# Performance work log

Measured on AMD Instinct MI355X. Metric: run time of the kernel, lower is better.

Reference implementation:

```python
import jax, jax.numpy as jnp
import numpy as np

KSIZE = 5      # equivalent steerable kernel size
KMAX = 3       # max circular harmonic
STRIDE = 2
N_IN, N_OUT = 32, 16
B_TOTAL = 3 + 2 * KMAX  # 3 radial atoms at k=0, 2 per harmonic k>=1


def _make_basis():
    # Radial steerable base: Gaussian rings x circular harmonics cos(k*theta)/sin(k*theta)
    ys, xs = np.mgrid[:KSIZE, :KSIZE].astype(np.float64) - (KSIZE - 1) / 2
    r = np.sqrt(xs ** 2 + ys ** 2)
    th = np.arctan2(ys, xs)
    ring = lambda r0: np.exp(-(r - r0) ** 2 / (2 * 0.6 ** 2))
    b0 = np.stack([ring(r0) for r0 in (0.0, 1.0, 2.0)])          # (3, 5, 5)
    br, bi = [], []
    for k in range(1, KMAX + 1):
        br.append(np.stack([ring(r0) * np.cos(k * th) for r0 in (1.0, 2.0)]))  # (2,5,5)
        bi.append(np.stack([ring(r0) * np.sin(k * th) for r0 in (1.0, 2.0)]))
    return (b0.astype(np.float32),
            [b.astype(np.float32) for b in br],
            [b.astype(np.float32) for b in bi])


def _conv_transpose(x, w):
    # torch conv_transpose2d (stride=2, padding='same' -> pad=2, output_padding=1)
    # == dilated-input conv with spatially flipped kernel, explicit pad (2,3).
    rhs = jnp.flip(w, axis=(2, 3))  # (o, i, kh, kw)
    return jax.lax.conv_general_dilated(
        x, rhs, window_strides=(1, 1), padding=((2, 3), (2, 3)),
        lhs_dilation=(STRIDE, STRIDE),
        dimension_numbers=('NCHW', 'OIHW', 'NCHW'))


def setup_inputs() -> dict:
    key = jax.random.key(0)
    k1, k2, k3, k4 = jax.random.split(key, 4)
    x = jax.random.normal(k1, (8, N_IN, 192, 192), jnp.float32)
    # alpha[0]=cos-like, alpha[1]=sin-like field at output resolution; not unit-norm,
    # rho is derived from its norm (rho=None path of forward()).
    alpha = jax.random.normal(k2, (2, 8, 1, 384, 384), jnp.float32)
    weights = jax.random.normal(k3, (N_OUT, N_IN, B_TOTAL), jnp.float32) / np.sqrt(N_IN * B_TOTAL)
    bias = jax.random.normal(k4, (N_OUT,), jnp.float32) * 0.05
    return {"x": x, "alpha": alpha, "weights": weights, "bias": bias}


def reference(x, alpha, weights, bias):
    b0, br, bi = _make_basis()
    # normalize_vector: rho = |alpha|, alpha <- alpha / rho
    rho = jnp.sqrt(jnp.sum(alpha * alpha, axis=0))          # (b, 1, Ho, Wo)
    au = alpha / (rho[None] + 1e-8)
    c1, s1 = au[0], au[1]                                    # cos(a), sin(a)
    # k=0 term (rotation invariant)
    out = _conv_transpose(x, jnp.einsum('oib,bhw->oihw', weights[:, :, :3], jnp.asarray(b0)))
    ck, sk = c1, s1
    off = 3
    for k in range(KMAX):  # harmonics k=1..KMAX, steered by cos(k a), sin(k a)
        wk = weights[:, :, off:off + 2]
        off += 2
        Kr = jnp.einsum('oib,bhw->oihw', wk, jnp.asarray(br[k]))
        Ki = jnp.einsum('oib,bhw->oihw', wk, jnp.asarray(bi[k]))
        out = out + _conv_transpose(x, Kr) * ck + _conv_transpose(x, Ki) * sk
        ckn = ck * c1 - sk * s1  # Chebyshev-style recurrence for cos/sin of (k+1)a
        skn = sk * c1 + ck * s1
        ck, sk = ckn, skn
    return rho * out + bias[None, :, None, None]
```

## Files before the change

### kernel.cpp

```cpp
#include <hip/hip_runtime.h>

#define HIN 192
#define WOUT 384
#define NIN 32
#define NOUT 16
#define NSLOT 9
#define HP 194
#define HPLANE (HP * HP)
#define HQBATCH ((size_t)HPLANE * 18)

typedef float v2f __attribute__((ext_vector_type(2)));

__device__ __forceinline__ unsigned short f2bf(float f) {
    union { float f; unsigned int u; } v; v.f = f;
    unsigned int r = v.u + 0x7fffu + ((v.u >> 16) & 1u);
    return (unsigned short)(r >> 16);
}
__device__ __forceinline__ v2f up2(unsigned u) {
    v2f r;
    r.x = __uint_as_float(u << 16);
    r.y = __uint_as_float(u & 0xffff0000u);
    return r;
}

__global__ __launch_bounds__(256) void kprep_w(const float* __restrict__ w, float* __restrict__ Wt) {
    int t = blockIdx.x * 256 + threadIdx.x;
    if (t >= NIN * NSLOT * NOUT) return;
    int c = t >> 8, r = t & 255;
    int i = r >> 3, j = r & 7;
    int m = c * 8 + j;
    int s = m >> 4, o = m & 15;
    Wt[t] = w[(o * NIN + i) * NSLOT + s];
}

__global__ __launch_bounds__(256) void kzero(uint4* __restrict__ hq, int nb) {
    int t = blockIdx.x * 256 + threadIdx.x;
    if (t >= nb * 772) return;
    int b = t / 772, r = t % 772;
    int iy, ix;
    if (r < 194)      { iy = 0;           ix = r; }
    else if (r < 388) { iy = 193;         ix = r - 194; }
    else if (r < 580) { iy = r - 388 + 1; ix = 0; }
    else              { iy = r - 580 + 1; ix = 193; }
    uint4* p = hq + (size_t)b * HQBATCH + iy * HP + ix;
    uint4 z; z.x = 0; z.y = 0; z.z = 0; z.w = 0;
    #pragma unroll
    for (int c = 0; c < 18; ++c) p[(size_t)c * HPLANE] = z;
}

__global__ __launch_bounds__(256) void kA(const float* __restrict__ x,
                                          const float* __restrict__ Wt,
                                          uint4* __restrict__ hq, int n0) {
    const int b = blockIdx.y;
    const int n = n0 + b;
    const int px = blockIdx.x * 256 + threadIdx.x;
    const int iy = px / HIN, ix = px % HIN;
    const float* xp = x + (size_t)n * NIN * HIN * HIN + px;
    float xv[NIN];
    #pragma unroll
    for (int i = 0; i < NIN; ++i) xv[i] = xp[(size_t)i * HIN * HIN];
    const int pos = (iy + 1) * HP + (ix + 1);
    uint4* hb = hq + (size_t)b * HQBATCH;
    #pragma unroll 1
    for (int c = 0; c < 18; ++c) {
        const float* wc = Wt + c * 256;
        float a[8];
        #pragma unroll
        for (int j = 0; j < 8; ++j) a[j] = 0.0f;
        #pragma unroll
        for (int i = 0; i < NIN; ++i) {
            const float xi = xv[i];
            #pragma unroll
            for (int j = 0; j < 8; ++j) a[j] = fmaf(wc[i * 8 + j], xi, a[j]);
        }
        uint4 v;
        v.x = (unsigned)f2bf(a[0]) | ((unsigned)f2bf(a[1]) << 16);
        v.y = (unsigned)f2bf(a[2]) | ((unsigned)f2bf(a[3]) << 16);
        v.z = (unsigned)f2bf(a[4]) | ((unsigned)f2bf(a[5]) << 16);
        v.w = (unsigned)f2bf(a[6]) | ((unsigned)f2bf(a[7]) << 16);
        hb[(size_t)c * HPLANE + pos] = v;
    }
}

template<int PY, int PX, int HF>
__device__ __forceinline__ void kb_body(const uint4* __restrict__ hb,
                                        const float* __restrict__ alpha,
                                        const float* __restrict__ bias_,
                                        float (&stage)[2][16][128],
                                        const float2 (&Cb)[NSLOT][25],
                                        int n, int Y, int X, int lane) {
    const int oy = 2 * Y + PY, ox = 2 * X + PX;
    const int aoff = (n * WOUT + oy) * WOUT + ox;
    const float a0 = alpha[aoff];
    const float a1 = alpha[(size_t)8 * WOUT * WOUT + aoff];
    const float rr = sqrtf(a0 * a0 + a1 * a1);
    const float inv = 1.0f / (rr + 1e-8f);
    float cc[3], ss[3];
    cc[0] = a0 * inv;                      ss[0] = a1 * inv;
    cc[1] = cc[0] * cc[0] - ss[0] * ss[0]; ss[1] = 2.0f * cc[0] * ss[0];
    cc[2] = cc[1] * cc[0] - ss[1] * ss[0]; ss[2] = ss[1] * cc[0] + cc[1] * ss[0];

    v2f acc2[4];
    #pragma unroll
    for (int j = 0; j < 4; ++j) { acc2[j].x = 0.0f; acc2[j].y = 0.0f; }

    #pragma unroll 1
    for (int ty = 0; ty < 3 - PY; ++ty) {
        const int piy = Y + 2 - ty;
        #pragma unroll 1
        for (int tx = 0; tx < 3 - PX; ++tx) {
            const int pix = X + 2 - tx;
            const int bi = (PY + 2 * ty) * 5 + (PX + 2 * tx);
            const unsigned pos = (unsigned)(piy * HP + pix);
            #pragma unroll
            for (int s = 0; s < NSLOT; ++s) {
                const float2 C = Cb[s][bi];
                float eb;
                if      (s < 3) eb = C.x;
                else if (s < 5) eb = C.x * cc[0] + C.y * ss[0];
                else if (s < 7) eb = C.x * cc[1] + C.y * ss[1];
                else            eb = C.x * cc[2] + C.y * ss[2];
                const uint4 v = hb[(size_t)(2 * s + HF) * HPLANE + pos];
                v2f e2; e2.x = eb; e2.y = eb;
                acc2[0] += e2 * up2(v.x);
                acc2[1] += e2 * up2(v.y);
                acc2[2] += e2 * up2(v.z);
                acc2[3] += e2 * up2(v.w);
            }
        }
    }

    #pragma unroll
    for (int j = 0; j < 4; ++j) {
        stage[PY][HF * 8 + 2 * j + 0][2 * lane + PX] = rr * acc2[j].x + bias_[HF * 8 + 2 * j + 0];
        stage[PY][HF * 8 + 2 * j + 1][2 * lane + PX] = rr * acc2[j].y + bias_[HF * 8 + 2 * j + 1];
    }
}

__global__ __launch_bounds__(512, 4) void kB(const uint4* __restrict__ hq,
                                             const float* __restrict__ alpha,
                                             const float* __restrict__ bias,
                                             float* __restrict__ out, int n0, int nb) {
    __shared__ float2 Cb[NSLOT][25];
    __shared__ float stage[2][16][128];
    {
        const int q = threadIdx.x;
        if (q < NSLOT * 25) {
            int s = q / 25, p = q % 25;
            int ky = p / 5, kx = p % 5;
            float ys = (float)(ky - 2), xs = (float)(kx - 2);
            float r = sqrtf(xs * xs + ys * ys);
            float th = atan2f(ys, xs);
            float cr, ci;
            if (s < 3) {
                float d = r - (float)s;
                cr = expf(-d * d * (1.0f / 0.72f));
                ci = 0.0f;
            } else {
                int k = (s - 3) / 2 + 1;
                float r0 = ((s - 3) & 1) ? 2.0f : 1.0f;
                float d = r - r0;
                float ring = expf(-d * d * (1.0f / 0.72f));
                float a = (float)k * th;
                cr = ring * cosf(a);
                ci = ring * sinf(a);
            }
            Cb[s][p] = make_float2(cr, ci);
        }
    }
    __syncthreads();

    const int tot = gridDim.x;
    const int cpx = tot >> 3;
    const int swz = ((int)blockIdx.x & 7) * cpx + ((int)blockIdx.x >> 3);
    const int Y = swz % 192;
    const int rest = swz / 192;
    const int b = rest % nb;
    const int bx = rest / nb;

    const int n = n0 + b;
    const int lane = threadIdx.x & 63;
    const int wv = threadIdx.x >> 6;
    const int X0 = bx * 64;
    const int X = X0 + lane;
    const uint4* hb = hq + (size_t)b * HQBATCH;

    switch (wv) {
        case 0: kb_body<0, 0, 0>(hb, alpha, bias, stage, Cb, n, Y, X, lane); break;
        case 1: kb_body<0, 1, 0>(hb, alpha, bias, stage, Cb, n, Y, X, lane); break;
        case 2: kb_body<1, 0, 0>(hb, alpha, bias, stage, Cb, n, Y, X, lane); break;
        case 3: kb_body<1, 1, 0>(hb, alpha, bias, stage, Cb, n, Y, X, lane); break;
        case 4: kb_body<0, 0, 1>(hb, alpha, bias, stage, Cb, n, Y, X, lane); break;
        case 5: kb_body<0, 1, 1>(hb, alpha, bias, stage, Cb, n, Y, X, lane); break;
        case 6: kb_body<1, 0, 1>(hb, alpha, bias, stage, Cb, n, Y, X, lane); break;
        default: kb_body<1, 1, 1>(hb, alpha, bias, stage, Cb, n, Y, X, lane); break;
    }

    __syncthreads();

    #pragma unroll
    for (int q = 0; q < 8; ++q) {
        const int f = q * 512 + threadIdx.x;
        const int row = f >> 7, col = f & 127;
        const int py = row >> 4, o = row & 15;
        out[(((size_t)n * NOUT + o) * WOUT + (2 * Y + py)) * WOUT + 2 * X0 + col]
            = stage[py][o][col];
    }
}

__global__ __launch_bounds__(256) void steered_convT(
    const float* __restrict__ x, const float* __restrict__ alpha,
    const float* __restrict__ weights, const float* __restrict__ bias,
    float* __restrict__ out) {
    __shared__ float sb[15 * 25];
    for (int q = threadIdx.x; q < 375; q += 256) {
        int s = q / 25, p = q % 25;
        int ky = p / 5, kx = p % 5;
        float ys = (float)(ky - 2), xs = (float)(kx - 2);
        float r = sqrtf(xs * xs + ys * ys);
        float th = atan2f(ys, xs);
        float val;
        if (s < 3) { float d = r - (float)s; val = expf(-d * d * (1.0f / 0.72f)); }
        else {
            int k = (s - 3) / 4 + 1; int rem = (s - 3) & 3;
            float r0 = (rem & 1) ? 2.0f : 1.0f; float d = r - r0;
            float ring = expf(-d * d * (1.0f / 0.72f));
            float ang = (float)k * th;
            val = ring * ((rem < 2) ? cosf(ang) : sinf(ang));
        }
        sb[q] = val;
    }
    __syncthreads();
    int idx = blockIdx.x * 256 + threadIdx.x;
    int ox = idx % WOUT; int tt = idx / WOUT; int oy = tt % WOUT; int n = tt / WOUT;
    const int plane = WOUT * WOUT;
    int aoff = (n * WOUT + oy) * WOUT + ox;
    float a0 = alpha[aoff], a1 = alpha[8 * plane + aoff];
    float rho = sqrtf(a0 * a0 + a1 * a1);
    float inv = 1.0f / (rho + 1e-8f);
    float c1 = a0 * inv, s1 = a1 * inv;
    float c2 = c1 * c1 - s1 * s1, s2 = 2.0f * s1 * c1;
    float c3 = c2 * c1 - s2 * s1, s3 = s2 * c1 + c2 * s1;
    int py = oy & 1, px = ox & 1;
    int iy0 = (oy >> 1) + 1, ix0 = (ox >> 1) + 1;
    float eb[9][9]; int off[9];
    #pragma unroll
    for (int t = 0; t < 9; ++t) {
        int ty = t / 3, tx = t % 3;
        int ky = py + 2 * ty, kx = px + 2 * tx;
        int iy = iy0 - ty, ix = ix0 - tx;
        bool v = (ky < 5) && (kx < 5) && (iy >= 0) && (iy < HIN) && (ix >= 0) && (ix < HIN);
        float m = v ? 1.0f : 0.0f;
        int ciy = min(max(iy, 0), HIN - 1), cix = min(max(ix, 0), HIN - 1);
        off[t] = ciy * HIN + cix;
        int bi_ = min(ky, 4) * 5 + min(kx, 4);
        eb[0][t] = sb[0 * 25 + bi_] * m;
        eb[1][t] = sb[1 * 25 + bi_] * m;
        eb[2][t] = sb[2 * 25 + bi_] * m;
        eb[3][t] = (sb[3 * 25 + bi_] * c1 + sb[5 * 25 + bi_] * s1) * m;
        eb[4][t] = (sb[4 * 25 + bi_] * c1 + sb[6 * 25 + bi_] * s1) * m;
        eb[5][t] = (sb[7 * 25 + bi_] * c2 + sb[9 * 25 + bi_] * s2) * m;
        eb[6][t] = (sb[8 * 25 + bi_] * c2 + sb[10 * 25 + bi_] * s2) * m;
        eb[7][t] = (sb[11 * 25 + bi_] * c3 + sb[13 * 25 + bi_] * s3) * m;
        eb[8][t] = (sb[12 * 25 + bi_] * c3 + sb[14 * 25 + bi_] * s3) * m;
    }
    float acc[NOUT];
    #pragma unroll
    for (int o = 0; o < NOUT; ++o) acc[o] = 0.0f;
    const float* xn = x + (size_t)n * NIN * HIN * HIN;
    for (int i = 0; i < NIN; ++i) {
        const float* xp = xn + (size_t)i * HIN * HIN;
        float tap[9];
        #pragma unroll
        for (int t = 0; t < 9; ++t) tap[t] = xp[off[t]];
        float G[9];
        #pragma unroll
        for (int b = 0; b < 9; ++b) {
            float s = 0.0f;
            #pragma unroll
            for (int t = 0; t < 9; ++t) s += eb[b][t] * tap[t];
            G[b] = s;
        }
        const float* wp = weights + i * 9;
        #pragma unroll
        for (int o = 0; o < NOUT; ++o) {
            float s = acc[o];
            #pragma unroll
            for (int b = 0; b < 9; ++b) s += wp[o * NIN * 9 + b] * G[b];
            acc[o] = s;
        }
    }
    #pragma unroll
    for (int o = 0; o < NOUT; ++o)
        out[((size_t)(n * NOUT + o) * WOUT + oy) * WOUT + ox] = rho * acc[o] + bias[o];
}

extern "C" void kernel_launch(void* const* d_in, const int* in_sizes, int n_in,
                              void* d_out, int out_size, void* d_ws, size_t ws_size,
                              hipStream_t stream) {
    const float* x       = (const float*)d_in[0];
    const float* alpha   = (const float*)d_in[1];
    const float* weights = (const float*)d_in[2];
    const float* bias    = (const float*)d_in[3];
    float* out = (float*)d_out;

    const size_t hoff = 32768;
    const size_t perb = HQBATCH * 16;
    int cb = 0;
    if (ws_size > hoff) cb = (int)((ws_size - hoff) / perb);
    if (cb > 8) cb = 8;

    if (cb < 1) {
        const int pixels = 8 * WOUT * WOUT;
        steered_convT<<<dim3(pixels / 256), 256, 0, stream>>>(x, alpha, weights, bias, out);
        return;
    }

    float* Wt = (float*)d_ws;
    uint4* hq = (uint4*)((char*)d_ws + hoff);

    kprep_w<<<dim3(18), 256, 0, stream>>>(weights, Wt);

    for (int n0 = 0; n0 < 8; n0 += cb) {
        int nb = 8 - n0; if (nb > cb) nb = cb;
        kzero<<<dim3((nb * 772 + 255) / 256), 256, 0, stream>>>(hq, nb);
        kA<<<dim3(144, nb), 256, 0, stream>>>(x, Wt, hq, n0);
        kB<<<dim3(576 * nb), 512, 0, stream>>>(hq, alpha, bias, out, n0, nb);
    }
}
```

Before: 154.2 us.

## Stage per-block halo tile of intermediate planes in LDS for transposed-conv gather

kB now cooperatively loads an 18-plane, 3-row, 66-column bf16 halo tile of the intermediate tensor into shared memory before the tap loop. The eight waves then read their shifted taps from LDS instead of re-fetching overlapping uint4 values from global/L2. This adds about 57 KB of LDS per block, which may lower occupancy below the launch-bounds target, plus an extra barrier. kA's channel-mixing FMAs are also rewritten as packed two-wide vector FMAs.

Measured after the change: 162.4 us. 5.3% more time.

```diff
diff --git a/kernel.cpp b/kernel.cpp
--- a/kernel.cpp
+++ b/kernel.cpp
@@ -8,6 +8,7 @@
 #define HP 194
 #define HPLANE (HP * HP)
 #define HQBATCH ((size_t)HPLANE * 18)
+#define NSTG (18 * 3 * 66)
 
 typedef float v2f __attribute__((ext_vector_type(2)));
 
@@ -64,26 +65,32 @@
     #pragma unroll 1
     for (int c = 0; c < 18; ++c) {
         const float* wc = Wt + c * 256;
-        float a[8];
-        #pragma unroll
-        for (int j = 0; j < 8; ++j) a[j] = 0.0f;
+        v2f a2[4];
+        #pragma unroll
+        for (int j = 0; j < 4; ++j) { a2[j].x = 0.0f; a2[j].y = 0.0f; }
         #pragma unroll
         for (int i = 0; i < NIN; ++i) {
             const float xi = xv[i];
+            v2f x2; x2.x = xi; x2.y = xi;
             #pragma unroll
-            for (int j = 0; j < 8; ++j) a[j] = fmaf(wc[i * 8 + j], xi, a[j]);
+            for (int j = 0; j < 4; ++j) {
+                v2f w2;
+                w2.x = wc[i * 8 + 2 * j];
+                w2.y = wc[i * 8 + 2 * j + 1];
+                a2[j] += w2 * x2;
+            }
         }
         uint4 v;
-        v.x = (unsigned)f2bf(a[0]) | ((unsigned)f2bf(a[1]) << 16);
-        v.y = (unsigned)f2bf(a[2]) | ((unsigned)f2bf(a[3]) << 16);
-        v.z = (unsigned)f2bf(a[4]) | ((unsigned)f2bf(a[5]) << 16);
-        v.w = (unsigned)f2bf(a[6]) | ((unsigned)f2bf(a[7]) << 16);
+        v.x = (unsigned)f2bf(a2[0].x) | ((unsigned)f2bf(a2[0].y) << 16);
+        v.y = (unsigned)f2bf(a2[1].x) | ((unsigned)f2bf(a2[1].y) << 16);
+        v.z = (unsigned)f2bf(a2[2].x) | ((unsigned)f2bf(a2[2].y) << 16);
+        v.w = (unsigned)f2bf(a2[3].x) | ((unsigned)f2bf(a2[3].y) << 16);
         hb[(size_t)c * HPLANE + pos] = v;
     }
 }
 
 template<int PY, int PX, int HF>
-__device__ __forceinline__ void kb_body(const uint4* __restrict__ hb,
+__device__ __forceinline__ void kb_body(const uint4* __restrict__ ringp,
                                         const float* __restrict__ alpha,
                                         const float* __restrict__ bias_,
                                         float (&stage)[2][16][128],
@@ -106,12 +113,10 @@
 
     #pragma unroll 1
     for (int ty = 0; ty < 3 - PY; ++ty) {
-        const int piy = Y + 2 - ty;
         #pragma unroll 1
         for (int tx = 0; tx < 3 - PX; ++tx) {
-            const int pix = X + 2 - tx;
             const int bi = (PY + 2 * ty) * 5 + (PX + 2 * tx);
-            const unsigned pos = (unsigned)(piy * HP + pix);
+            const uint4* rp = ringp + HF * 198 + (2 - ty) * 66 + (lane + 2 - tx);
             #pragma unroll
             for (int s = 0; s < NSLOT; ++s) {
                 const float2 C = Cb[s][bi];
@@ -120,7 +125,7 @@
                 else if (s < 5) eb = C.x * cc[0] + C.y * ss[0];
                 else if (s < 7) eb = C.x * cc[1] + C.y * ss[1];
                 else            eb = C.x * cc[2] + C.y * ss[2];
-                const uint4 v = hb[(size_t)(2 * s + HF) * HPLANE + pos];
+                const uint4 v = rp[s * 396];
                 v2f e2; e2.x = eb; e2.y = eb;
                 acc2[0] += e2 * up2(v.x);
                 acc2[1] += e2 * up2(v.y);
@@ -142,6 +147,7 @@
                                              const float* __restrict__ bias,
                                              float* __restrict__ out, int n0, int nb) {
     __shared__ float2 Cb[NSLOT][25];
+    __shared__ __align__(16) uint4 ring[NSTG];
     __shared__ float stage[2][16][128];
     {
         const int q = threadIdx.x;
@@ -160,15 +166,14 @@
                 int k = (s - 3) / 2 + 1;
                 float r0 = ((s - 3) & 1) ? 2.0f : 1.0f;
                 float d = r - r0;
-                float ring = expf(-d * d * (1.0f / 0.72f));
+                float rg = expf(-d * d * (1.0f / 0.72f));
                 float a = (float)k * th;
-                cr = ring * cosf(a);
-                ci = ring * sinf(a);
+                cr = rg * cosf(a);
+                ci = rg * sinf(a);
             }
             Cb[s][p] = make_float2(cr, ci);
         }
     }
-    __syncthreads();
 
     const int tot = gridDim.x;
     const int cpx = tot >> 3;
@@ -185,15 +190,24 @@
     const int X = X0 + lane;
     const uint4* hb = hq + (size_t)b * HQBATCH;
 
+    for (int it = threadIdx.x; it < NSTG; it += 512) {
+        const int pl = it / 198;
+        const int rm = it - pl * 198;
+        const int row = rm / 66;
+        const int pos = rm - row * 66;
+        ring[it] = hb[(size_t)pl * HPLANE + (size_t)(Y + row) * HP + X0 + pos];
+    }
+    __syncthreads();
+
     switch (wv) {
-        case 0: kb_body<0, 0, 0>(hb, alpha, bias, stage, Cb, n, Y, X, lane); break;
-        case 1: kb_body<0, 1, 0>(hb, alpha, bias, stage, Cb, n, Y, X, lane); break;
-        case 2: kb_body<1, 0, 0>(hb, alpha, bias, stage, Cb, n, Y, X, lane); break;
-        case 3: kb_body<1, 1, 0>(hb, alpha, bias, stage, Cb, n, Y, X, lane); break;
-        case 4: kb_body<0, 0, 1>(hb, alpha, bias, stage, Cb, n, Y, X, lane); break;
-        case 5: kb_body<0, 1, 1>(hb, alpha, bias, stage, Cb, n, Y, X, lane); break;
-        case 6: kb_body<1, 0, 1>(hb, alpha, bias, stage, Cb, n, Y, X, lane); break;
-        default: kb_body<1, 1, 1>(hb, alpha, bias, stage, Cb, n, Y, X, lane); break;
+        case 0: kb_body<0, 0, 0>(ring, alpha, bias, stage, Cb, n, Y, X, lane); break;
+        case 1: kb_body<0, 1, 0>(ring, alpha, bias, stage, Cb, n, Y, X, lane); break;
+        case 2: kb_body<1, 0, 0>(ring, alpha, bias, stage, Cb, n, Y, X, lane); break;
+        case 3: kb_body<1, 1, 0>(ring, alpha, bias, stage, Cb, n, Y, X, lane); break;
+        case 4: kb_body<0, 0, 1>(ring, alpha, bias, stage, Cb, n, Y, X, lane); break;
+        case 5: kb_body<0, 1, 1>(ring, alpha, bias, stage, Cb, n, Y, X, lane); break;
+        case 6: kb_body<1, 0, 1>(ring, alpha, bias, stage, Cb, n, Y, X, lane); break;
+        default: kb_body<1, 1, 1>(ring, alpha, bias, stage, Cb, n, Y, X, lane); break;
     }
 
     __syncthreads();
```
